# Kernel tuning notes

Measured on AMD Instinct MI355X. Metric: run time of the kernel, lower is better.

## Reference

```python
import jax, jax.numpy as jnp
import numpy as np

WS = 16                     # window_size
OW = 24                     # overlap_win_size = int(16*0.5)+16
PAD = (OW - WS) // 2        # unfold padding = 4
DIM = 384
HEADS = 6
HID = 768                   # mlp_ratio 2.0 * dim
TABLE = (WS + OW - 1) ** 2  # 1521


def _rel_pos_index():
    ch = np.arange(WS)
    coords = np.stack(np.meshgrid(ch, ch, indexing='ij')).reshape(2, -1)      # (2, WS*WS)
    co = np.arange(OW)
    coords_o = np.stack(np.meshgrid(co, co, indexing='ij')).reshape(2, -1)    # (2, OW*OW)
    rel = coords[:, :, None] - coords_o[:, None, :]                           # (2, nq, nk)
    rel = rel.transpose(1, 2, 0).astype(np.int64)
    rel[..., 0] += OW - 1
    rel[..., 1] += OW - 1
    rel[..., 0] *= WS + OW - 1
    return rel.sum(-1)                                                        # (WS*WS, OW*OW)

RPI = jnp.asarray(_rel_pos_index())


def _ln(x, g, b, eps=1e-5):
    m = x.mean(-1, keepdims=True)
    v = ((x - m) ** 2).mean(-1, keepdims=True)
    return (x - m) / jnp.sqrt(v + eps) * g + b


def _overlap_windows(t, H, W):
    # t: (B,H,W,C) -> (B*nw, OW*OW, C); overlapping patches, stride WS, pad PAD
    B, _, _, C = t.shape
    nH, nW = H // WS, W // WS
    tp = jnp.pad(t, ((0, 0), (PAD, PAD), (PAD, PAD), (0, 0)))
    r = (jnp.arange(nH) * WS)[:, None] + jnp.arange(OW)   # (nH, OW)
    c = (jnp.arange(nW) * WS)[:, None] + jnp.arange(OW)   # (nW, OW)
    p = tp[:, r]              # (B, nH, OW, Wp, C)
    p = p[:, :, :, c]         # (B, nH, OW, nW, OW, C)
    p = p.transpose(0, 1, 3, 2, 4, 5).reshape(B * nH * nW, OW * OW, C)
    return p


def setup_inputs() -> dict:
    key = jax.random.key(0)
    ks = jax.random.split(key, 8)
    H = W = 192
    B = 1
    inp = {
        'x': jax.random.normal(ks[0], (B, H * W, DIM), dtype=jnp.float32),
        'norm1_g': jnp.ones((DIM,), jnp.float32),
        'norm1_b': jnp.zeros((DIM,), jnp.float32),
        'qkv_w': jax.random.normal(ks[1], (DIM, 3 * DIM), jnp.float32) * 0.02,
        'qkv_b': jnp.zeros((3 * DIM,), jnp.float32),
        'rpb_table': jax.random.normal(ks[2], (TABLE, HEADS), jnp.float32) * 0.02,
        'proj_w': jax.random.normal(ks[3], (DIM, DIM), jnp.float32) * 0.02,
        'proj_b': jnp.zeros((DIM,), jnp.float32),
        'norm2_g': jnp.ones((DIM,), jnp.float32),
        'norm2_b': jnp.zeros((DIM,), jnp.float32),
        'fc1_w': jax.random.normal(ks[4], (DIM, HID), jnp.float32) * 0.02,
        'fc1_b': jnp.zeros((HID,), jnp.float32),
        'fc2_w': jax.random.normal(ks[5], (HID, DIM), jnp.float32) * 0.02,
        'fc2_b': jnp.zeros((DIM,), jnp.float32),
        'H': H,
        'W': W,
    }
    return inp


def reference(x, norm1_g, norm1_b, qkv_w, qkv_b, rpb_table, proj_w, proj_b,
              norm2_g, norm2_b, fc1_w, fc1_b, fc2_w, fc2_b, H, W):
    B, L, C = x.shape
    d = C // HEADS
    scale = d ** (-0.5)
    nH, nW = H // WS, W // WS

    shortcut = x
    xn = _ln(x, norm1_g, norm1_b).reshape(B, H, W, C)
    qkv = xn @ qkv_w + qkv_b                                   # (B,H,W,3C)
    q, k, v = qkv[..., :C], qkv[..., C:2 * C], qkv[..., 2 * C:]

    # non-overlapping query windows: (B*nw, WS*WS, C)
    qw = q.reshape(B, nH, WS, nW, WS, C).transpose(0, 1, 3, 2, 4, 5).reshape(-1, WS * WS, C)
    # overlapping key/value windows: (B*nw, OW*OW, C)
    kw = _overlap_windows(k, H, W)
    vw = _overlap_windows(v, H, W)

    b_ = qw.shape[0]
    qh = qw.reshape(b_, WS * WS, HEADS, d) * scale
    kh = kw.reshape(b_, OW * OW, HEADS, d)
    vh = vw.reshape(b_, OW * OW, HEADS, d)

    attn = jnp.einsum('bqhd,bkhd->bhqk', qh, kh)               # (b_, H, nq, nk)
    bias = rpb_table[RPI].transpose(2, 0, 1)                   # (heads, nq, nk)
    attn = jax.nn.softmax(attn + bias[None], axis=-1)
    out = jnp.einsum('bhqk,bkhd->bqhd', attn, vh).reshape(b_, WS * WS, C)

    # window reverse -> (B, H*W, C)
    out = out.reshape(B, nH, nW, WS, WS, C).transpose(0, 1, 3, 2, 4, 5).reshape(B, H * W, C)
    out = out @ proj_w + proj_b

    x = shortcut + out
    h = _ln(x, norm2_g, norm2_b)
    h = jax.nn.gelu(h @ fc1_w + fc1_b, approximate=False)
    h = h @ fc2_w + fc2_b
    return x + h
```

## Files before the change

kernel.cpp:

```cpp
#include <hip/hip_runtime.h>

#define LTOK 36864
#define DIMC 384
#define NHEADS 6
#define HDIM 64
#define HIDD 768
#define NWIN 12
#define WSZ 16
#define OWS 24
#define KVTOK 576

using bf16x8 = __attribute__((ext_vector_type(8))) short;
using f32x4  = __attribute__((ext_vector_type(4))) float;

__device__ inline unsigned short f2bf(float f) {
  unsigned u = __float_as_uint(f);
  return (unsigned short)((u + 0x7FFFu + ((u >> 16) & 1u)) >> 16);
}
__device__ __forceinline__ unsigned cvt_pk_bf16(float lo, float hi) {
  unsigned r;
  asm volatile("v_cvt_pk_bf16_f32 %0, %1, %2" : "=v"(r) : "v"(lo), "v"(hi));
  return r;
}
__device__ __forceinline__ unsigned short f2bf1(float x) {
  return (unsigned short)(cvt_pk_bf16(x, x) & 0xffffu);
}
__device__ __forceinline__ float fexp2(float x) {
#if __has_builtin(__builtin_amdgcn_exp2f)
  return __builtin_amdgcn_exp2f(x);
#else
  return exp2f(x);
#endif
}

typedef __attribute__((address_space(1))) const unsigned int GAS_U32;
typedef __attribute__((address_space(3))) unsigned int LAS_U32;
__device__ __forceinline__ void gl16(const void* g, void* l) {
  __builtin_amdgcn_global_load_lds((GAS_U32*)g, (LAS_U32*)l, 16, 0, 0);
}

__global__ void convt_kernel(const float* __restrict__ w, unsigned short* __restrict__ wt,
                             int K, int N) {
  int id = blockIdx.x * 256 + threadIdx.x;
  if (id >= K * N) return;
  int n = id / K;
  int k = id - n * K;
  wt[id] = f2bf(w[(size_t)k * N + n]);
}

__global__ void rpb_expand_kernel(const float* __restrict__ rpb, float* __restrict__ biasm8) {
  int id = blockIdx.x * 256 + threadIdx.x;
  if (id >= NHEADS * 256 * 576) return;
  int head = id / 147456;
  int rem = id - head * 147456;
  int q = rem / 576;
  int kt = rem - q * 576;
  int ty = q >> 4, tx = q & 15;
  int oy = kt / 24, ox = kt - (kt / 24) * 24;
  biasm8[id] = rpb[((ty - oy + 23) * 39 + (tx - ox + 23)) * NHEADS + head] * 8.0f;
}

__global__ __launch_bounds__(256) void ln_kernel(const float* __restrict__ x,
                                                 const float* __restrict__ g,
                                                 const float* __restrict__ b,
                                                 unsigned short* __restrict__ out) {
  int row = blockIdx.x * 4 + (threadIdx.x >> 6);
  int lane = threadIdx.x & 63;
  const float* xr = x + (size_t)row * DIMC;
  float v[6];
  float s = 0.f, ss = 0.f;
#pragma unroll
  for (int i = 0; i < 6; ++i) {
    v[i] = xr[lane + i * 64];
    s += v[i];
    ss += v[i] * v[i];
  }
#pragma unroll
  for (int off = 32; off; off >>= 1) {
    s += __shfl_xor(s, off);
    ss += __shfl_xor(ss, off);
  }
  float mean = s * (1.f / DIMC);
  float var = ss * (1.f / DIMC) - mean * mean;
  float rstd = rsqrtf(var + 1e-5f);
  unsigned short* outr = out + (size_t)row * DIMC;
#pragma unroll
  for (int i = 0; i < 6; ++i) {
    int c = lane + i * 64;
    outr[c] = f2bf((v[i] - mean) * rstd * g[c] + b[c]);
  }
}

template <int EPI>
__global__ __launch_bounds__(256) void gemm_bf16(const unsigned short* __restrict__ A,
                                                 const unsigned short* __restrict__ Bt,
                                                 const float* __restrict__ bias,
                                                 const float* __restrict__ resid,
                                                 void* __restrict__ outv,
                                                 int M, int N, int K) {
  __shared__ unsigned short As[2][4096];
  __shared__ unsigned short Bs[2][4096];
  const int tid = threadIdx.x;
  int id = blockIdx.y * gridDim.x + blockIdx.x;
  int chunk = (gridDim.x * gridDim.y) >> 3;
  int lid = (id & 7) * chunk + (id >> 3);
  const int m0 = (lid / gridDim.x) * 128;
  const int n0 = (lid % gridDim.x) * 128;
  const int lane = tid & 63;
  const int wave = tid >> 6;
  const int wr = wave >> 1;
  const int wc = wave & 1;
  const int l15 = lane & 15, l4 = lane >> 4;

  f32x4 acc[4][4];
#pragma unroll
  for (int i = 0; i < 4; ++i)
#pragma unroll
    for (int j = 0; j < 4; ++j) acc[i][j] = (f32x4){0.f, 0.f, 0.f, 0.f};

  const int srow = tid >> 2;
  const int scol = (tid & 3) << 3;
  const unsigned short* ga = A + (size_t)(m0 + srow) * K + scol;
  const unsigned short* gb = Bt + (size_t)(n0 + srow) * K + scol;

#define STAGE(buf, k0)                                        \
  do {                                                        \
    unsigned short* lA = As[buf] + wave * 512;                \
    unsigned short* lB = Bs[buf] + wave * 512;                \
    gl16(ga + (k0), lA);                                      \
    gl16(ga + (size_t)64 * K + (k0), lA + 2048);              \
    gl16(gb + (k0), lB);                                      \
    gl16(gb + (size_t)64 * K + (k0), lB + 2048);              \
  } while (0)

  STAGE(0, 0);
  __syncthreads();

  const int nt = K >> 5;
  for (int t = 0; t < nt; ++t) {
    const int cur = t & 1;
    if (t + 1 < nt) STAGE(cur ^ 1, (t + 1) * 32);

    const unsigned short* arp = As[cur] + (wr * 64 + l15) * 32 + l4 * 8;
    const unsigned short* brp = Bs[cur] + (wc * 64 + l15) * 32 + l4 * 8;
    bf16x8 af[4], bfr[4];
#pragma unroll
    for (int i = 0; i < 4; ++i) af[i] = *(const bf16x8*)(arp + i * 512);
#pragma unroll
    for (int j = 0; j < 4; ++j) bfr[j] = *(const bf16x8*)(brp + j * 512);
#pragma unroll
    for (int i = 0; i < 4; ++i)
#pragma unroll
      for (int j = 0; j < 4; ++j)
        acc[i][j] = __builtin_amdgcn_mfma_f32_16x16x32_bf16(af[i], bfr[j], acc[i][j], 0, 0, 0);

    __syncthreads();
  }
#undef STAGE

#pragma unroll
  for (int j = 0; j < 4; ++j) {
    int gcol = n0 + wc * 64 + j * 16 + l15;
    float bv = bias[gcol];
#pragma unroll
    for (int i = 0; i < 4; ++i) {
#pragma unroll
      for (int r = 0; r < 4; ++r) {
        int grow = m0 + wr * 64 + i * 16 + l4 * 4 + r;
        float v = acc[i][j][r] + bv;
        size_t idx = (size_t)grow * N + gcol;
        if (EPI == 0) {
          ((unsigned short*)outv)[idx] = f2bf(v);
        } else if (EPI == 1) {
          ((float*)outv)[idx] = resid[idx] + v;
        } else {
          float gv = 0.5f * v * (1.f + erff(v * 0.70710678118654752f));
          ((unsigned short*)outv)[idx] = f2bf(gv);
        }
      }
    }
  }
}

__global__ __launch_bounds__(256, 3) void attn_kernel(const unsigned short* __restrict__ qkv,
                                                      const float* __restrict__ biasm8,
                                                      unsigned short* __restrict__ att) {
  __shared__ unsigned short ks[2][64][72];
  __shared__ unsigned short vts[2][64][72];
  __shared__ unsigned short pt[4][32][40];
  int bid = blockIdx.x;
  int lid = (bid & 7) * 216 + (bid >> 3);
  const int hw = lid >> 1;
  const int qh = lid & 1;
  const int win = hw / NHEADS;
  const int head = hw - win * NHEADS;
  const int wy = win / NWIN, wx = win - (win / NWIN) * NWIN;
  const int tid = threadIdx.x;
  const int w = tid >> 6, lane = tid & 63;
  const int l15 = lane & 15, l4 = lane >> 4;
  const float SC02 = 0.125f * 1.44269504f;
  const float C0 = -8.f * 1.44269504f;

  const int qrow0 = qh * 128 + w * 32;

  bf16x8 qf[2][2];
#pragma unroll
  for (int jq = 0; jq < 2; ++jq) {
    int q = qrow0 + jq * 16 + l15;
    int gy = wy * WSZ + (q >> 4), gx = wx * WSZ + (q & 15);
    const unsigned short* qp = qkv + (size_t)(gy * 192 + gx) * 1152 + head * HDIM + l4 * 8;
    qf[jq][0] = *(const bf16x8*)qp;
    qf[jq][1] = *(const bf16x8*)(qp + 32);
  }

  const float* bias_base = biasm8 + (size_t)head * 147456 + (size_t)(qrow0 + l15) * 576 + l4 * 4;

#define KS_W(buf, k0v, k1v)                          \
  do {                                               \
    *(uint4*)&ks[buf][lane][w * 16] = (k0v);         \
    *(uint4*)&ks[buf][lane][w * 16 + 8] = (k1v);     \
  } while (0)
#define VTS_W(buf, v0v, v1v)                                           \
  do {                                                                 \
    const unsigned short* vv = (const unsigned short*)&(v0v);          \
    _Pragma("unroll") for (int j = 0; j < 8; ++j)                      \
        vts[buf][w * 16 + j][lane] = vv[j];                            \
    vv = (const unsigned short*)&(v1v);                                \
    _Pragma("unroll") for (int j = 0; j < 8; ++j)                      \
        vts[buf][w * 16 + 8 + j][lane] = vv[j];                        \
  } while (0)

  {
    int kt = lane;
    int oy = kt / OWS, ox = kt - (kt / OWS) * OWS;
    int gy = wy * WSZ + oy - 4, gx = wx * WSZ + ox - 4;
    uint4 k0 = {0,0,0,0}, k1 = {0,0,0,0}, v0 = {0,0,0,0}, v1 = {0,0,0,0};
    if ((unsigned)gy < 192u && (unsigned)gx < 192u) {
      const unsigned short* gp = qkv + (size_t)(gy * 192 + gx) * 1152 + DIMC + head * HDIM + w * 16;
      k0 = *(const uint4*)gp;         k1 = *(const uint4*)(gp + 8);
      v0 = *(const uint4*)(gp + 384); v1 = *(const uint4*)(gp + 392);
    }
    KS_W(0, k0, k1);
    VTS_W(0, v0, v1);
  }

  f32x4 sacc[4][2];
#pragma unroll
  for (int i = 0; i < 4; ++i)
#pragma unroll
    for (int j2 = 0; j2 < 2; ++j2)
      sacc[i][j2] = *(const f32x4*)(bias_base + j2 * (16 * 576) + i * 16);

  __syncthreads();

  f32x4 oacc[2][4];
#pragma unroll
  for (int i = 0; i < 2; ++i)
#pragma unroll
    for (int j = 0; j < 4; ++j) oacc[i][j] = (f32x4){0.f, 0.f, 0.f, 0.f};
  float plsum[2] = {0.f, 0.f};

  for (int kb = 0; kb < 9; ++kb) {
    const int cur = kb & 1;
    const bool have = kb < 8;
    uint4 pk0 = {0,0,0,0}, pk1 = {0,0,0,0}, pv0 = {0,0,0,0}, pv1 = {0,0,0,0};
    if (have) {
      int kt = (kb + 1) * 64 + lane;
      int oy = kt / OWS, ox = kt - (kt / OWS) * OWS;
      int gy = wy * WSZ + oy - 4, gx = wx * WSZ + ox - 4;
      if ((unsigned)gy < 192u && (unsigned)gx < 192u) {
        const unsigned short* gp = qkv + (size_t)(gy * 192 + gx) * 1152 + DIMC + head * HDIM + w * 16;
        pk0 = *(const uint4*)gp;         pk1 = *(const uint4*)(gp + 8);
        pv0 = *(const uint4*)(gp + 384); pv1 = *(const uint4*)(gp + 392);
      }
    }

#pragma unroll
    for (int kk = 0; kk < 2; ++kk) {
      bf16x8 kf[4];
#pragma unroll
      for (int i = 0; i < 4; ++i)
        kf[i] = *(const bf16x8*)&ks[cur][i * 16 + l15][kk * 32 + l4 * 8];
      __builtin_amdgcn_s_setprio(1);
#pragma unroll
      for (int i = 0; i < 4; ++i)
#pragma unroll
        for (int j2 = 0; j2 < 2; ++j2)
          sacc[i][j2] = __builtin_amdgcn_mfma_f32_16x16x32_bf16(kf[i], qf[j2][kk], sacc[i][j2], 0, 0, 0);
      __builtin_amdgcn_s_setprio(0);
    }

#pragma unroll
    for (int i = 0; i < 4; ++i)
#pragma unroll
      for (int j2 = 0; j2 < 2; ++j2)
#pragma unroll
        for (int r = 0; r < 4; ++r) {
          float p = fexp2(fmaf(sacc[i][j2][r], SC02, C0));
          sacc[i][j2][r] = p;
          plsum[j2] += p;
        }

#pragma unroll
    for (int kk = 0; kk < 2; ++kk) {
#pragma unroll
      for (int i2 = 0; i2 < 2; ++i2)
#pragma unroll
        for (int j2 = 0; j2 < 2; ++j2) {
          int i = kk * 2 + i2;
          uint2 pk;
          pk.x = cvt_pk_bf16(sacc[i][j2][0], sacc[i][j2][1]);
          pk.y = cvt_pk_bf16(sacc[i][j2][2], sacc[i][j2][3]);
          *(uint2*)&pt[w][j2 * 16 + l15][i2 * 16 + l4 * 4] = pk;
        }
      bf16x8 pf[2], vf[4];
#pragma unroll
      for (int j2 = 0; j2 < 2; ++j2)
        pf[j2] = *(const bf16x8*)&pt[w][j2 * 16 + l15][l4 * 8];
#pragma unroll
      for (int jd = 0; jd < 4; ++jd)
        vf[jd] = *(const bf16x8*)&vts[cur][jd * 16 + l15][kk * 32 + l4 * 8];
      __builtin_amdgcn_s_setprio(1);
#pragma unroll
      for (int j2 = 0; j2 < 2; ++j2)
#pragma unroll
        for (int jd = 0; jd < 4; ++jd)
          oacc[j2][jd] = __builtin_amdgcn_mfma_f32_16x16x32_bf16(pf[j2], vf[jd], oacc[j2][jd], 0, 0, 0);
      __builtin_amdgcn_s_setprio(0);
    }

    if (have) {
      KS_W(cur ^ 1, pk0, pk1);
      VTS_W(cur ^ 1, pv0, pv1);
      const float* bp = bias_base + (kb + 1) * 64;
#pragma unroll
      for (int i = 0; i < 4; ++i)
#pragma unroll
        for (int j2 = 0; j2 < 2; ++j2)
          sacc[i][j2] = *(const f32x4*)(bp + j2 * (16 * 576) + i * 16);
    }
    __syncthreads();
  }
#undef KS_W
#undef VTS_W

  float invl[2];
#pragma unroll
  for (int j2 = 0; j2 < 2; ++j2) {
    plsum[j2] += __shfl_xor(plsum[j2], 16);
    plsum[j2] += __shfl_xor(plsum[j2], 32);
    invl[j2] = 1.f / plsum[j2];
  }

#pragma unroll
  for (int j2 = 0; j2 < 2; ++j2) {
#pragma unroll
    for (int r = 0; r < 4; ++r) {
      float il = __shfl(invl[j2], l4 * 4 + r);
      int q = qrow0 + j2 * 16 + l4 * 4 + r;
      int gy = wy * WSZ + (q >> 4), gx = wx * WSZ + (q & 15);
      unsigned short* op = att + (size_t)(gy * 192 + gx) * DIMC + head * HDIM + l15;
#pragma unroll
      for (int jd = 0; jd < 4; ++jd) op[jd * 16] = f2bf1(oacc[j2][jd][r] * il);
    }
  }
}

extern "C" void kernel_launch(void* const* d_in, const int* in_sizes, int n_in,
                              void* d_out, int out_size, void* d_ws, size_t ws_size,
                              hipStream_t stream) {
  const float* x      = (const float*)d_in[0];
  const float* n1g    = (const float*)d_in[1];
  const float* n1b    = (const float*)d_in[2];
  const float* qkv_w  = (const float*)d_in[3];
  const float* qkv_b  = (const float*)d_in[4];
  const float* rpb    = (const float*)d_in[5];
  const float* proj_w = (const float*)d_in[6];
  const float* proj_b = (const float*)d_in[7];
  const float* n2g    = (const float*)d_in[8];
  const float* n2b    = (const float*)d_in[9];
  const float* fc1_w  = (const float*)d_in[10];
  const float* fc1_b  = (const float*)d_in[11];
  const float* fc2_w  = (const float*)d_in[12];
  const float* fc2_b  = (const float*)d_in[13];
  float* out = (float*)d_out;

  char* ws = (char*)d_ws;
  unsigned short* xn   = (unsigned short*)ws;
  unsigned short* qkvb = (unsigned short*)(ws + 28311552);
  unsigned short* att  = (unsigned short*)(ws + 28311552 + 84934656);
  unsigned short* wq   = (unsigned short*)(ws + 141557760);
  unsigned short* wp   = wq + 1152 * 384;
  unsigned short* w1   = wp + 384 * 384;
  unsigned short* w2   = w1 + 768 * 384;
  float* biasm8 = (float*)ws;

  convt_kernel<<<(DIMC * 3 * DIMC + 255) / 256, 256, 0, stream>>>(qkv_w, wq, DIMC, 3 * DIMC);
  convt_kernel<<<(DIMC * DIMC + 255) / 256, 256, 0, stream>>>(proj_w, wp, DIMC, DIMC);
  convt_kernel<<<(DIMC * HIDD + 255) / 256, 256, 0, stream>>>(fc1_w, w1, DIMC, HIDD);
  convt_kernel<<<(HIDD * DIMC + 255) / 256, 256, 0, stream>>>(fc2_w, w2, HIDD, DIMC);

  ln_kernel<<<LTOK / 4, 256, 0, stream>>>(x, n1g, n1b, xn);
  gemm_bf16<0><<<dim3(1152 / 128, LTOK / 128), 256, 0, stream>>>(xn, wq, qkv_b, nullptr, qkvb,
                                                                 LTOK, 1152, DIMC);
  rpb_expand_kernel<<<(NHEADS * 256 * 576 + 255) / 256, 256, 0, stream>>>(rpb, biasm8);
  attn_kernel<<<dim3(NHEADS * 144 * 2), 256, 0, stream>>>(qkvb, biasm8, att);
  gemm_bf16<1><<<dim3(DIMC / 128, LTOK / 128), 256, 0, stream>>>(att, wp, proj_b, x, out,
                                                                 LTOK, DIMC, DIMC);
  ln_kernel<<<LTOK / 4, 256, 0, stream>>>(out, n2g, n2b, xn);
  gemm_bf16<2><<<dim3(HIDD / 128, LTOK / 128), 256, 0, stream>>>(xn, w1, fc1_b, nullptr, qkvb,
                                                                 LTOK, HIDD, DIMC);
  gemm_bf16<1><<<dim3(DIMC / 128, LTOK / 128), 256, 0, stream>>>(qkvb, w2, fc2_b, out, out,
                                                                 LTOK, DIMC, HIDD);
}
```

Before: 334.2 us.

## Double GEMM K-tile to 64 and merge weight-conversion launches into one

The bf16 GEMM now stages a 64-wide K slice per iteration instead of 32. LDS buffers double and the load mapping is rearranged so each wave fetches 8 rows of 64 columns. This halves the number of barrier and prefetch iterations per tile, at the cost of twice the LDS, which may reduce occupancy. The four weight transpose/convert launches are also fused into a single prep kernel to cut launch overhead.

```diff
diff --git a/kernel.cpp b/kernel.cpp
--- a/kernel.cpp
+++ b/kernel.cpp
@@ -39,13 +39,27 @@
   __builtin_amdgcn_global_load_lds((GAS_U32*)g, (LAS_U32*)l, 16, 0, 0);
 }
 
-__global__ void convt_kernel(const float* __restrict__ w, unsigned short* __restrict__ wt,
-                             int K, int N) {
+__global__ void prep_kernel(const float* __restrict__ qkv_w, const float* __restrict__ proj_w,
+                            const float* __restrict__ fc1_w, const float* __restrict__ fc2_w,
+                            unsigned short* __restrict__ wq, unsigned short* __restrict__ wp,
+                            unsigned short* __restrict__ w1, unsigned short* __restrict__ w2) {
   int id = blockIdx.x * 256 + threadIdx.x;
-  if (id >= K * N) return;
-  int n = id / K;
-  int k = id - n * K;
-  wt[id] = f2bf(w[(size_t)k * N + n]);
+  if (id < 442368) {
+    int n = id / 384, k = id - n * 384;
+    wq[id] = f2bf(qkv_w[(size_t)k * 1152 + n]);
+  } else if (id < 589824) {
+    int i = id - 442368;
+    int n = i / 384, k = i - n * 384;
+    wp[i] = f2bf(proj_w[(size_t)k * 384 + n]);
+  } else if (id < 884736) {
+    int i = id - 589824;
+    int n = i / 384, k = i - n * 384;
+    w1[i] = f2bf(fc1_w[(size_t)k * 768 + n]);
+  } else {
+    int i = id - 884736;
+    int n = i / 768, k = i - n * 768;
+    w2[i] = f2bf(fc2_w[(size_t)k * 384 + n]);
+  }
 }
 
 __global__ void rpb_expand_kernel(const float* __restrict__ rpb, float* __restrict__ biasm8) {
@@ -98,8 +112,8 @@
                                                  const float* __restrict__ resid,
                                                  void* __restrict__ outv,
                                                  int M, int N, int K) {
-  __shared__ unsigned short As[2][4096];
-  __shared__ unsigned short Bs[2][4096];
+  __shared__ unsigned short As[2][8192];
+  __shared__ unsigned short Bs[2][8192];
   const int tid = threadIdx.x;
   int id = blockIdx.y * gridDim.x + blockIdx.x;
   int chunk = (gridDim.x * gridDim.y) >> 3;
@@ -118,41 +132,42 @@
 #pragma unroll
     for (int j = 0; j < 4; ++j) acc[i][j] = (f32x4){0.f, 0.f, 0.f, 0.f};
 
-  const int srow = tid >> 2;
-  const int scol = (tid & 3) << 3;
+  const int srow = wave * 8 + (lane >> 3);
+  const int scol = (lane & 7) << 3;
   const unsigned short* ga = A + (size_t)(m0 + srow) * K + scol;
   const unsigned short* gb = Bt + (size_t)(n0 + srow) * K + scol;
 
-#define STAGE(buf, k0)                                        \
-  do {                                                        \
-    unsigned short* lA = As[buf] + wave * 512;                \
-    unsigned short* lB = Bs[buf] + wave * 512;                \
-    gl16(ga + (k0), lA);                                      \
-    gl16(ga + (size_t)64 * K + (k0), lA + 2048);              \
-    gl16(gb + (k0), lB);                                      \
-    gl16(gb + (size_t)64 * K + (k0), lB + 2048);              \
+#define STAGE(buf, k0)                                                     \
+  do {                                                                     \
+    _Pragma("unroll") for (int p = 0; p < 4; ++p) {                        \
+      gl16(ga + (size_t)(p * 32) * K + (k0), As[buf] + p * 2048 + wave * 512); \
+      gl16(gb + (size_t)(p * 32) * K + (k0), Bs[buf] + p * 2048 + wave * 512); \
+    }                                                                      \
   } while (0)
 
   STAGE(0, 0);
   __syncthreads();
 
-  const int nt = K >> 5;
+  const int nt = K >> 6;
   for (int t = 0; t < nt; ++t) {
     const int cur = t & 1;
-    if (t + 1 < nt) STAGE(cur ^ 1, (t + 1) * 32);
-
-    const unsigned short* arp = As[cur] + (wr * 64 + l15) * 32 + l4 * 8;
-    const unsigned short* brp = Bs[cur] + (wc * 64 + l15) * 32 + l4 * 8;
-    bf16x8 af[4], bfr[4];
-#pragma unroll
-    for (int i = 0; i < 4; ++i) af[i] = *(const bf16x8*)(arp + i * 512);
-#pragma unroll
-    for (int j = 0; j < 4; ++j) bfr[j] = *(const bf16x8*)(brp + j * 512);
-#pragma unroll
-    for (int i = 0; i < 4; ++i)
-#pragma unroll
-      for (int j = 0; j < 4; ++j)
-        acc[i][j] = __builtin_amdgcn_mfma_f32_16x16x32_bf16(af[i], bfr[j], acc[i][j], 0, 0, 0);
+    if (t + 1 < nt) STAGE(cur ^ 1, (t + 1) * 64);
+
+#pragma unroll
+    for (int kk = 0; kk < 2; ++kk) {
+      const char* ab = (const char*)As[cur] + (wr * 64 + l15) * 128 + kk * 64 + l4 * 16;
+      const char* bb = (const char*)Bs[cur] + (wc * 64 + l15) * 128 + kk * 64 + l4 * 16;
+      bf16x8 af[4], bfr[4];
+#pragma unroll
+      for (int i = 0; i < 4; ++i) af[i] = *(const bf16x8*)(ab + i * 2048);
+#pragma unroll
+      for (int j = 0; j < 4; ++j) bfr[j] = *(const bf16x8*)(bb + j * 2048);
+#pragma unroll
+      for (int i = 0; i < 4; ++i)
+#pragma unroll
+        for (int j = 0; j < 4; ++j)
+          acc[i][j] = __builtin_amdgcn_mfma_f32_16x16x32_bf16(af[i], bfr[j], acc[i][j], 0, 0, 0);
+    }
 
     __syncthreads();
   }
@@ -395,10 +410,7 @@
   unsigned short* w2   = w1 + 768 * 384;
   float* biasm8 = (float*)ws;
 
-  convt_kernel<<<(DIMC * 3 * DIMC + 255) / 256, 256, 0, stream>>>(qkv_w, wq, DIMC, 3 * DIMC);
-  convt_kernel<<<(DIMC * DIMC + 255) / 256, 256, 0, stream>>>(proj_w, wp, DIMC, DIMC);
-  convt_kernel<<<(DIMC * HIDD + 255) / 256, 256, 0, stream>>>(fc1_w, w1, DIMC, HIDD);
-  convt_kernel<<<(HIDD * DIMC + 255) / 256, 256, 0, stream>>>(fc2_w, w2, HIDD, DIMC);
+  prep_kernel<<<4608, 256, 0, stream>>>(qkv_w, proj_w, fc1_w, fc2_w, wq, wp, w1, w2);
 
   ln_kernel<<<LTOK / 4, 256, 0, stream>>>(x, n1g, n1b, xn);
   gemm_bf16<0><<<dim3(1152 / 128, LTOK / 128), 256, 0, stream>>>(xn, wq, qkv_b, nullptr, qkvb,
```

Result: slower. 344.2 us (+3.0%).
